# Kernel optimization log

Measured on AMD Instinct MI355X. Metric: run time of the kernel, lower is better.

The kernel has to match this reference:

```python
import jax, jax.numpy as jnp
import numpy as np

SEQ, BATCH, IN_DIM, HID_DIM = 512, 256, 256, 256
NQ = 8
ALPHA = 0.5
MLP_HID = 128


def _linear_init(key, fan_in, fan_out):
    k1, k2 = jax.random.split(key)
    bound = 1.0 / np.sqrt(fan_in)
    W = jax.random.uniform(k1, (fan_in, fan_out), minval=-bound, maxval=bound, dtype=jnp.float32)
    b = jax.random.uniform(k2, (fan_out,), minval=-bound, maxval=bound, dtype=jnp.float32)
    return W, b


def setup_inputs() -> dict:
    key = jax.random.key(0)
    ks = jax.random.split(key, 12)
    cdim = IN_DIM + HID_DIM
    inputs = jax.random.normal(ks[0], (SEQ, BATCH, IN_DIM), dtype=jnp.float32)
    W1, b1 = _linear_init(ks[1], cdim, MLP_HID)
    W2, b2 = _linear_init(ks[2], MLP_HID, NQ * 4)
    Wf, bf = _linear_init(ks[3], cdim, 1)
    Wi, bi = _linear_init(ks[4], cdim, 1)
    Wg, bg = _linear_init(ks[5], cdim, 1)
    Wo, bo = _linear_init(ks[6], cdim, 1)
    rzf = jax.random.normal(ks[7], (NQ,), dtype=jnp.float32)
    rzi = jax.random.normal(ks[8], (NQ,), dtype=jnp.float32)
    rzg = jax.random.normal(ks[9], (NQ,), dtype=jnp.float32)
    rzo = jax.random.normal(ks[10], (NQ,), dtype=jnp.float32)
    return dict(inputs=inputs, W1=W1, b1=b1, W2=W2, b2=b2,
                Wf=Wf, bf=bf, Wi=Wi, bi=bi, Wg=Wg, bg=bg, Wo=Wo, bo=bo,
                rzf=rzf, rzi=rzi, rzg=rzg, rzo=rzo)


def _qgate(theta):
    # Analytic expectations of the RX/RZ/CNOT-chain circuit:
    # <Z_k> = prod_{j<=k} cos(theta_j); rz_params cancel in Z expectations.
    # Returns mean over wires, shape (batch, 1).
    return jnp.mean(jnp.cumprod(jnp.cos(theta), axis=-1), axis=-1, keepdims=True)


def reference(inputs, W1, b1, W2, b2, Wf, bf, Wi, bi, Wg, bg, Wo, bo, rzf, rzi, rzg, rzo):
    batch = inputs.shape[1]
    hx0 = jnp.zeros((batch, HID_DIM), dtype=inputs.dtype)
    cx0 = jnp.zeros((batch, HID_DIM), dtype=inputs.dtype)

    def step(carry, x):
        hx, cx = carry
        combined = jnp.concatenate([x, hx], axis=1)  # (B, in+hid)
        f_c = jax.nn.sigmoid(combined @ Wf + bf)
        i_c = jax.nn.sigmoid(combined @ Wi + bi)
        g_c = jnp.tanh(combined @ Wg + bg)
        o_c = jax.nn.sigmoid(combined @ Wo + bo)
        h1 = jax.nn.relu(combined @ W1 + b1)
        q = h1 @ W2 + b2  # (B, 4*NQ)
        q_f = _qgate(q[:, 0 * NQ:1 * NQ])
        q_i = _qgate(q[:, 1 * NQ:2 * NQ])
        q_g = _qgate(q[:, 2 * NQ:3 * NQ])
        q_o = _qgate(q[:, 3 * NQ:4 * NQ])
        f = (1 - ALPHA) * f_c + ALPHA * jax.nn.sigmoid(q_f)
        i = (1 - ALPHA) * i_c + ALPHA * jax.nn.sigmoid(q_i)
        g = (1 - ALPHA) * g_c + ALPHA * jnp.tanh(q_g)
        o = (1 - ALPHA) * o_c + ALPHA * jax.nn.sigmoid(q_o)
        cx_new = f * cx + i * g
        hx_new = o * jnp.tanh(cx_new)
        return (hx_new, cx_new), hx_new

    (hx, cx), outputs = jax.lax.scan(step, (hx0, cx0), inputs)
    return outputs, (hx, cx)
```

## Files before the change

### kernel.cpp

```cpp
#include <hip/hip_runtime.h>

#define SEQ 512
#define BATCH 256
#define INDIM 256
#define MLP 128
#define M_ROWS (SEQ * BATCH)
#define PRE_STRIDE 136
#define AUX_OFF ((size_t)M_ROWS * PRE_STRIDE)

#define BT_OFF (AUX_OFF + 160)

typedef __attribute__((ext_vector_type(8))) short short8v;
typedef __attribute__((ext_vector_type(4))) float f32x4;

__device__ __forceinline__ unsigned short bf16_rtne(float f) {
  unsigned u = __float_as_uint(f);
  unsigned r = u + 0x7FFFu + ((u >> 16) & 1u);
  return (unsigned short)(r >> 16);
}
__device__ __forceinline__ void cvt2(float f, unsigned short& h,
                                     unsigned short& l) {
  h = bf16_rtne(f);
  l = bf16_rtne(f - __uint_as_float((unsigned)h << 16));
}

__global__ __launch_bounds__(256) void prep_kernel(
    const float* __restrict__ W1,
    const float* __restrict__ Wf, const float* __restrict__ Wi,
    const float* __restrict__ Wg, const float* __restrict__ Wo,
    const float* __restrict__ bf, const float* __restrict__ bi,
    const float* __restrict__ bg, const float* __restrict__ bo,
    const float* __restrict__ b1, float* __restrict__ aux,
    float* __restrict__ btbase) {
  const int tid = threadIdx.x;
  const int blk = blockIdx.x;
  unsigned short* bth = (unsigned short*)btbase;
  unsigned short* btl = (unsigned short*)(btbase + 18432);
  float* b144 = btbase + 36864;

  if (blk == 0) {
    if (tid < 128) {
      float s = 0.f;
      for (int k = 0; k < 256; ++k) s += W1[(size_t)(256 + k) * 128 + tid];
      aux[tid] = s;
    } else if (tid < 132) {
      const int g = tid - 128;
      const float* w = (g == 0) ? Wf : (g == 1) ? Wi : (g == 2) ? Wg : Wo;
      float s = 0.f;
      for (int k = 0; k < 256; ++k) s += w[256 + k];
      aux[128 + g] = s;
    } else if (tid < 136) {
      const int g = tid - 132;
      const float* bp = (g == 0) ? bf : (g == 1) ? bi : (g == 2) ? bg : bo;
      aux[132 + g] = bp[0];
    }
    if (tid < 144) {
      const float bv = (tid < 128) ? b1[tid]
                     : (tid == 128) ? bf[0] : (tid == 129) ? bi[0]
                     : (tid == 130) ? bg[0] : (tid == 131) ? bo[0] : 0.f;
      b144[tid] = bv;
    }
  } else if (blk == 1) {
    for (int idx = tid; idx < 1024; idx += 256) {
      const int n = 128 + (idx >> 8), k = idx & 255;
      const float* wg = (n == 128) ? Wf : (n == 129) ? Wi
                       : (n == 130) ? Wg : Wo;
      unsigned short h, l;
      cvt2(wg[k], h, l);
      bth[n * 256 + k] = h;
      btl[n * 256 + k] = l;
    }
    for (int idx = tid; idx < 3072; idx += 256) {
      const int n = 132 + (idx >> 8), k = idx & 255;
      bth[n * 256 + k] = 0;
      btl[n * 256 + k] = 0;
    }
  } else {
    const int k = 2 * (blk - 2) + (tid >> 7);
    const int n = tid & 127;
    unsigned short h, l;
    cvt2(W1[(size_t)k * 128 + n], h, l);
    bth[n * 256 + k] = h;
    btl[n * 256 + k] = l;
  }
}

__global__ __attribute__((amdgpu_waves_per_eu(1, 4))) __launch_bounds__(256)
void gemm_kernel(const float* __restrict__ X,
                 const unsigned short* __restrict__ Bth,
                 const unsigned short* __restrict__ Btl,
                 const float* __restrict__ bias144,
                 float* __restrict__ PRE) {
  __shared__ __align__(16) unsigned short Ah[2048];
  __shared__ __align__(16) unsigned short Al[2048];
  __shared__ __align__(16) unsigned short Bh[4608];
  __shared__ __align__(16) unsigned short Bl[4608];

  const int tid = threadIdx.x;
  const size_t rowbase = (size_t)blockIdx.x * 64;
  const int lane = tid & 63, wv = tid >> 6;
  const int l15 = lane & 15, kgl = lane >> 4;

  f32x4 acc[9];
#pragma unroll
  for (int nt = 0; nt < 9; ++nt) acc[nt] = (f32x4){0.f, 0.f, 0.f, 0.f};

  for (int kc = 0; kc < 256; kc += 32) {
    __syncthreads();
    {
      const int r = tid >> 2, kg = tid & 3;
      const float4 xa = *(const float4*)&X[(rowbase + r) * 256 + kc + kg * 8];
      const float4 xb =
          *(const float4*)&X[(rowbase + r) * 256 + kc + kg * 8 + 4];
      unsigned short h0, h1, h2, h3, h4, h5, h6, h7;
      unsigned short l0, l1, l2, l3, l4, l5, l6, l7;
      cvt2(xa.x, h0, l0); cvt2(xa.y, h1, l1);
      cvt2(xa.z, h2, l2); cvt2(xa.w, h3, l3);
      cvt2(xb.x, h4, l4); cvt2(xb.y, h5, l5);
      cvt2(xb.z, h6, l6); cvt2(xb.w, h7, l7);
      const short8v hv = {(short)h0, (short)h1, (short)h2, (short)h3,
                          (short)h4, (short)h5, (short)h6, (short)h7};
      const short8v lv = {(short)l0, (short)l1, (short)l2, (short)l3,
                          (short)l4, (short)l5, (short)l6, (short)l7};
      const int dst = (((r >> 4) * 4 + kg) * 16 + (r & 15)) * 8;
      *(short8v*)&Ah[dst] = hv;
      *(short8v*)&Al[dst] = lv;
    }
#pragma unroll
    for (int s = 0; s < 3; ++s) {
      const int tau = tid + s * 256;
      if (tau < 576) {
        const int n = tau >> 2, kg = tau & 3;
        const int src = n * 256 + kc + kg * 8;
        const int dst = (((n >> 4) * 4 + kg) * 16 + (n & 15)) * 8;
        *(short8v*)&Bh[dst] = *(const short8v*)&Bth[src];
        *(short8v*)&Bl[dst] = *(const short8v*)&Btl[src];
      }
    }
    __syncthreads();

    const int ab = ((wv * 4 + kgl) * 16 + l15) * 8;
    const short8v ah = *(const short8v*)&Ah[ab];
    const short8v al = *(const short8v*)&Al[ab];
#pragma unroll
    for (int nt = 0; nt < 9; ++nt) {
      const int bb = ((nt * 4 + kgl) * 16 + l15) * 8;
      const short8v bh = *(const short8v*)&Bh[bb];
      const short8v bl = *(const short8v*)&Bl[bb];
      acc[nt] = __builtin_amdgcn_mfma_f32_16x16x32_bf16(ah, bh, acc[nt], 0, 0, 0);
      acc[nt] = __builtin_amdgcn_mfma_f32_16x16x32_bf16(ah, bl, acc[nt], 0, 0, 0);
      acc[nt] = __builtin_amdgcn_mfma_f32_16x16x32_bf16(al, bh, acc[nt], 0, 0, 0);
    }
  }

#pragma unroll
  for (int nt = 0; nt < 9; ++nt) {
    const int col = nt * 16 + l15;
    if (col < 132) {
      const float bb = bias144[col];
#pragma unroll
      for (int q = 0; q < 4; ++q) {
        PRE[(rowbase + wv * 16 + kgl * 4 + q) * PRE_STRIDE + col] =
            acc[nt][q] + bb;
      }
    }
  }
}

__device__ __forceinline__ float sigmoid_f(float x) {
  return __fdividef(1.0f, 1.0f + __expf(-x));
}
__device__ __forceinline__ float tanh_f(float x) {
  const float e = __expf(-2.0f * x);
  return __fdividef(1.0f - e, 1.0f + e);
}
__device__ __forceinline__ float readlane_f(float v, int lane) {
  return __int_as_float(__builtin_amdgcn_readlane(__float_as_int(v), lane));
}

__global__ __attribute__((amdgpu_waves_per_eu(1, 1))) __launch_bounds__(64)
void rec_kernel(
    const float* __restrict__ PRE, const float* __restrict__ W2,
    const float* __restrict__ b2, const float* __restrict__ aux,
    float* __restrict__ out) {
  __shared__ __align__(16) float h1s[128];

  const int l = threadIdx.x;
  const int b = blockIdx.x;
  const int m = l & 31, half = l >> 5;
  const int g = m >> 3;
  const int g8 = g * 8;

  float w2r[64];
#pragma unroll
  for (int u = 0; u < 64; ++u) w2r[u] = W2[(size_t)(half * 64 + u) * 32 + m];
  const float b2m = b2[m];
  const float2 s1 = *(const float2*)&aux[2 * l];
  const float4 sg = *(const float4*)&aux[128];

  float h = 0.f, c = 0.f;

  const float* pr0 = PRE + (size_t)b * PRE_STRIDE;
  const size_t ts = (size_t)BATCH * PRE_STRIDE;

  float2 p0 = *(const float2*)(pr0 + 0 * ts + 2 * l);
  float4 g0 = *(const float4*)(pr0 + 0 * ts + 128);
  float2 p1 = *(const float2*)(pr0 + 1 * ts + 2 * l);
  float4 g1 = *(const float4*)(pr0 + 1 * ts + 128);

  const float4* h1p = (const float4*)&h1s[half * 64];

  for (int t = 0; t < SEQ; ++t) {
    const float h10 = fmaxf(fmaf(h, s1.x, p0.x), 0.f);
    const float h11 = fmaxf(fmaf(h, s1.y, p0.y), 0.f);

    ((float2*)h1s)[l] = make_float2(h10, h11);
    asm volatile("" ::: "memory");

    const float zf = fmaf(h, sg.x, g0.x);
    const float zi = fmaf(h, sg.y, g0.y);
    const float zg = fmaf(h, sg.z, g0.z);
    const float zo = fmaf(h, sg.w, g0.w);
    const float cf = sigmoid_f(zf);
    const float ci = sigmoid_f(zi);
    const float cg = tanh_f(zg);
    const float co = sigmoid_f(zo);
    p0 = p1; g0 = g1;
    const int tn = (t + 2 < SEQ) ? (t + 2) : (SEQ - 1);
    p1 = *(const float2*)(pr0 + (size_t)tn * ts + 2 * l);
    g1 = *(const float4*)(pr0 + (size_t)tn * ts + 128);

    float q0 = 0.f, q1 = 0.f, q2 = 0.f, q3 = 0.f;
#pragma unroll
    for (int jj = 0; jj < 16; ++jj) {
      const float4 hv = h1p[jj];
      q0 = fmaf(hv.x, w2r[4 * jj + 0], q0);
      q1 = fmaf(hv.y, w2r[4 * jj + 1], q1);
      q2 = fmaf(hv.z, w2r[4 * jj + 2], q2);
      q3 = fmaf(hv.w, w2r[4 * jj + 3], q3);
    }
    const float part = (q0 + q1) + (q2 + q3);

    const float full = part + __shfl_xor(part, 32, 64);
    const float cm = __cosf(full + b2m);
    const int sb = (l & 32) + g8;
    const float e0 = __shfl(cm, sb + 0, 64);
    const float e1 = __shfl(cm, sb + 1, 64);
    const float e2 = __shfl(cm, sb + 2, 64);
    const float e3 = __shfl(cm, sb + 3, 64);
    const float e4 = __shfl(cm, sb + 4, 64);
    const float e5 = __shfl(cm, sb + 5, 64);
    const float e6 = __shfl(cm, sb + 6, 64);
    const float e7 = __shfl(cm, sb + 7, 64);
    float p = e0, s = e0;
    p *= e1; s += p;
    p *= e2; s += p;
    p *= e3; s += p;
    p *= e4; s += p;
    p *= e5; s += p;
    p *= e6; s += p;
    p *= e7; s += p;
    const float qv = s * 0.125f;

    const float qarg = (g == 2) ? (2.0f * qv) : qv;
    const float qs = sigmoid_f(qarg);
    const float av = (g == 2) ? (2.0f * qs - 1.0f) : qs;

    const float aF = readlane_f(av, 0);
    const float aI = readlane_f(av, 8);
    const float aG = readlane_f(av, 16);
    const float aO = readlane_f(av, 24);

    const float f  = 0.5f * (cf + aF);
    const float ii = 0.5f * (ci + aI);
    const float gg = 0.5f * (cg + aG);
    const float oo = 0.5f * (co + aO);

    c = fmaf(f, c, ii * gg);
    h = oo * tanh_f(c);

    float4 hv4o; hv4o.x = h; hv4o.y = h; hv4o.z = h; hv4o.w = h;
    *(float4*)(out + ((size_t)t * BATCH + b) * 256 + 4 * l) = hv4o;
  }

  float4 hq; hq.x = h; hq.y = h; hq.z = h; hq.w = h;
  float4 cq; cq.x = c; cq.y = c; cq.z = c; cq.w = c;
  *(float4*)(out + (size_t)SEQ * BATCH * 256 + (size_t)b * 256 + 4 * l) = hq;
  *(float4*)(out + (size_t)SEQ * BATCH * 256 + (size_t)BATCH * 256 +
             (size_t)b * 256 + 4 * l) = cq;
}

extern "C" void kernel_launch(void* const* d_in, const int* in_sizes, int n_in,
                              void* d_out, int out_size, void* d_ws,
                              size_t ws_size, hipStream_t stream) {
  const float* X  = (const float*)d_in[0];
  const float* W1 = (const float*)d_in[1];
  const float* b1 = (const float*)d_in[2];
  const float* W2 = (const float*)d_in[3];
  const float* b2 = (const float*)d_in[4];
  const float* Wf = (const float*)d_in[5];
  const float* bf = (const float*)d_in[6];
  const float* Wi = (const float*)d_in[7];
  const float* bi = (const float*)d_in[8];
  const float* Wg = (const float*)d_in[9];
  const float* bg = (const float*)d_in[10];
  const float* Wo = (const float*)d_in[11];
  const float* bo = (const float*)d_in[12];

  float* ws  = (float*)d_ws;
  float* PRE = ws;
  float* aux = ws + AUX_OFF;
  float* btbase = ws + BT_OFF;
  const unsigned short* bth = (const unsigned short*)btbase;
  const unsigned short* btl = (const unsigned short*)(btbase + 18432);
  const float* b144 = btbase + 36864;
  float* out = (float*)d_out;

  prep_kernel<<<130, 256, 0, stream>>>(W1, Wf, Wi, Wg, Wo, bf, bi, bg, bo,
                                       b1, aux, btbase);
  gemm_kernel<<<M_ROWS / 64, 256, 0, stream>>>(X, bth, btl, b144, PRE);
  rec_kernel<<<BATCH, 64, 0, stream>>>(PRE, W2, b2, aux, out);
}
```

Measured before the change: 704.0 us.

## Pre-swizzle B into MFMA fragment layout and drop LDS staging in GEMM

The prep kernel now writes the bf16 hi/lo weight matrices directly in the per-lane MFMA fragment order, so the GEMM kernel can load B fragments straight from global memory with one coalesced vector load per lane. The A operand is also loaded and split per lane directly from global memory. Together these remove shared-memory staging and the two barriers per K-chunk. In exchange, every wave reloads B from global/L2 instead of sharing it through LDS, which raises cache traffic.

```diff
diff --git a/kernel.cpp b/kernel.cpp
--- a/kernel.cpp
+++ b/kernel.cpp
@@ -22,6 +22,11 @@
                                      unsigned short& l) {
   h = bf16_rtne(f);
   l = bf16_rtne(f - __uint_as_float((unsigned)h << 16));
+}
+__device__ __forceinline__ int frag_idx(int n, int k) {
+  const int nt = n >> 4, l15 = n & 15;
+  const int ch = k >> 5, kg = (k >> 3) & 3, j = k & 7;
+  return ((ch * 9 + nt) * 64 + kg * 16 + l15) * 8 + j;
 }
 
 __global__ __launch_bounds__(256) void prep_kernel(
@@ -67,21 +72,24 @@
                        : (n == 130) ? Wg : Wo;
       unsigned short h, l;
       cvt2(wg[k], h, l);
-      bth[n * 256 + k] = h;
-      btl[n * 256 + k] = l;
+      const int fi = frag_idx(n, k);
+      bth[fi] = h;
+      btl[fi] = l;
     }
     for (int idx = tid; idx < 3072; idx += 256) {
       const int n = 132 + (idx >> 8), k = idx & 255;
-      bth[n * 256 + k] = 0;
-      btl[n * 256 + k] = 0;
+      const int fi = frag_idx(n, k);
+      bth[fi] = 0;
+      btl[fi] = 0;
     }
   } else {
     const int k = 2 * (blk - 2) + (tid >> 7);
     const int n = tid & 127;
     unsigned short h, l;
     cvt2(W1[(size_t)k * 128 + n], h, l);
-    bth[n * 256 + k] = h;
-    btl[n * 256 + k] = l;
+    const int fi = frag_idx(n, k);
+    bth[fi] = h;
+    btl[fi] = l;
   }
 }
 
@@ -91,62 +99,35 @@
                  const unsigned short* __restrict__ Btl,
                  const float* __restrict__ bias144,
                  float* __restrict__ PRE) {
-  __shared__ __align__(16) unsigned short Ah[2048];
-  __shared__ __align__(16) unsigned short Al[2048];
-  __shared__ __align__(16) unsigned short Bh[4608];
-  __shared__ __align__(16) unsigned short Bl[4608];
-
   const int tid = threadIdx.x;
-  const size_t rowbase = (size_t)blockIdx.x * 64;
   const int lane = tid & 63, wv = tid >> 6;
   const int l15 = lane & 15, kgl = lane >> 4;
+  const size_t rowbase = (size_t)blockIdx.x * 64;
+  const size_t arow = rowbase + wv * 16 + l15;
 
   f32x4 acc[9];
 #pragma unroll
   for (int nt = 0; nt < 9; ++nt) acc[nt] = (f32x4){0.f, 0.f, 0.f, 0.f};
 
-  for (int kc = 0; kc < 256; kc += 32) {
-    __syncthreads();
-    {
-      const int r = tid >> 2, kg = tid & 3;
-      const float4 xa = *(const float4*)&X[(rowbase + r) * 256 + kc + kg * 8];
-      const float4 xb =
-          *(const float4*)&X[(rowbase + r) * 256 + kc + kg * 8 + 4];
-      unsigned short h0, h1, h2, h3, h4, h5, h6, h7;
-      unsigned short l0, l1, l2, l3, l4, l5, l6, l7;
-      cvt2(xa.x, h0, l0); cvt2(xa.y, h1, l1);
-      cvt2(xa.z, h2, l2); cvt2(xa.w, h3, l3);
-      cvt2(xb.x, h4, l4); cvt2(xb.y, h5, l5);
-      cvt2(xb.z, h6, l6); cvt2(xb.w, h7, l7);
-      const short8v hv = {(short)h0, (short)h1, (short)h2, (short)h3,
-                          (short)h4, (short)h5, (short)h6, (short)h7};
-      const short8v lv = {(short)l0, (short)l1, (short)l2, (short)l3,
-                          (short)l4, (short)l5, (short)l6, (short)l7};
-      const int dst = (((r >> 4) * 4 + kg) * 16 + (r & 15)) * 8;
-      *(short8v*)&Ah[dst] = hv;
-      *(short8v*)&Al[dst] = lv;
-    }
-#pragma unroll
-    for (int s = 0; s < 3; ++s) {
-      const int tau = tid + s * 256;
-      if (tau < 576) {
-        const int n = tau >> 2, kg = tau & 3;
-        const int src = n * 256 + kc + kg * 8;
-        const int dst = (((n >> 4) * 4 + kg) * 16 + (n & 15)) * 8;
-        *(short8v*)&Bh[dst] = *(const short8v*)&Bth[src];
-        *(short8v*)&Bl[dst] = *(const short8v*)&Btl[src];
-      }
-    }
-    __syncthreads();
-
-    const int ab = ((wv * 4 + kgl) * 16 + l15) * 8;
-    const short8v ah = *(const short8v*)&Ah[ab];
-    const short8v al = *(const short8v*)&Al[ab];
+#pragma unroll
+  for (int ch = 0; ch < 8; ++ch) {
+    const float4 xa = *(const float4*)&X[arow * 256 + ch * 32 + kgl * 8];
+    const float4 xb = *(const float4*)&X[arow * 256 + ch * 32 + kgl * 8 + 4];
+    unsigned short h0, h1, h2, h3, h4, h5, h6, h7;
+    unsigned short l0, l1, l2, l3, l4, l5, l6, l7;
+    cvt2(xa.x, h0, l0); cvt2(xa.y, h1, l1);
+    cvt2(xa.z, h2, l2); cvt2(xa.w, h3, l3);
+    cvt2(xb.x, h4, l4); cvt2(xb.y, h5, l5);
+    cvt2(xb.z, h6, l6); cvt2(xb.w, h7, l7);
+    const short8v ah = {(short)h0, (short)h1, (short)h2, (short)h3,
+                        (short)h4, (short)h5, (short)h6, (short)h7};
+    const short8v al = {(short)l0, (short)l1, (short)l2, (short)l3,
+                        (short)l4, (short)l5, (short)l6, (short)l7};
 #pragma unroll
     for (int nt = 0; nt < 9; ++nt) {
-      const int bb = ((nt * 4 + kgl) * 16 + l15) * 8;
-      const short8v bh = *(const short8v*)&Bh[bb];
-      const short8v bl = *(const short8v*)&Bl[bb];
+      const int fi = ((ch * 9 + nt) * 64 + lane) * 8;
+      const short8v bh = *(const short8v*)&Bth[fi];
+      const short8v bl = *(const short8v*)&Btl[fi];
       acc[nt] = __builtin_amdgcn_mfma_f32_16x16x32_bf16(ah, bh, acc[nt], 0, 0, 0);
       acc[nt] = __builtin_amdgcn_mfma_f32_16x16x32_bf16(ah, bl, acc[nt], 0, 0, 0);
       acc[nt] = __builtin_amdgcn_mfma_f32_16x16x32_bf16(al, bh, acc[nt], 0, 0, 0);
```

Measured after the change: 723.2 us. 1.03x slower.
